# Kernel tuning notes

Hardware: AMD Instinct MI355X
Metric: run time of the kernel (lower is better)

## Reference

```python
import jax, jax.numpy as jnp
import numpy as np

B, N_ATOMS, N_ALIGN = 65536, 128, 64


def setup_inputs() -> dict:
    key = jax.random.key(0)
    k1, k2 = jax.random.split(key)
    traj = jax.random.normal(k1, (B, N_ATOMS, 3), dtype=jnp.float32)
    ref_pos = jax.random.normal(k2, (N_ATOMS, 3), dtype=jnp.float32)
    align_idx = jnp.arange(N_ALIGN, dtype=jnp.int32)  # 0-based (ids - 1)
    return {"traj": traj, "ref_pos": ref_pos, "align_idx": align_idx}


def reference(traj, ref_pos, align_idx):
    # --- __init__: centered reference coordinates of alignment atoms ---
    ref_x = ref_pos[align_idx]                      # [K, 3]
    ref_x = ref_x - jnp.mean(ref_x, axis=0)         # center

    # --- forward: Kabsch alignment per frame ---
    sel = traj[:, align_idx, :]                     # [B, K, 3]
    x_c = jnp.mean(sel, axis=1, keepdims=True)      # [B, 1, 3]
    x_notran = sel - x_c                            # [B, K, 3]
    # xtmp = x_notran^T  -> prod[b] = x_notran[b]^T @ ref_x : [B, 3, 3]
    prod = jnp.einsum('bki,kj->bij', x_notran, ref_x)

    u, s, vh = jnp.linalg.svd(prod)                 # u,vh: [B, 3, 3]
    sign_vec = jnp.sign(jnp.linalg.det(u @ vh))     # [B]
    # diag(1, 1, sign) applied on the right of u
    d = jnp.stack([jnp.ones_like(sign_vec), jnp.ones_like(sign_vec), sign_vec], axis=-1)
    rotate_mat = (u * d[:, None, :]) @ vh           # [B, 3, 3]

    aligned_traj = jnp.matmul(traj - x_c, rotate_mat)  # [B, N, 3]
    return aligned_traj
```

## Files before the change

### kernel.cpp

```cpp
#include <hip/hip_runtime.h>
#include <math.h>

#define NATOMS 128
#define NALIGN 64
#define FPB    32
#define TPB    256

#define JACOBI_ROT(app, aqq, apq, arp, arq, pcol, qcol)                 \
  {                                                                     \
    float _apq = (apq);                                                 \
    if (fabsf(_apq) > 1e-20f) {                                         \
      float _tau = ((aqq) - (app)) / (2.0f * _apq);                     \
      float _t = (_tau >= 0.0f ? 1.0f : -1.0f) /                        \
                 (fabsf(_tau) + sqrtf(1.0f + _tau * _tau));             \
      float _c = rsqrtf(1.0f + _t * _t);                                \
      float _s = _t * _c;                                               \
      (app) -= _t * _apq;                                               \
      (aqq) += _t * _apq;                                               \
      (apq) = 0.0f;                                                     \
      float _rp = (arp), _rq = (arq);                                   \
      (arp) = _c * _rp - _s * _rq;                                      \
      (arq) = _s * _rp + _c * _rq;                                      \
      _Pragma("unroll")                                                 \
      for (int _r = 0; _r < 3; _r++) {                                  \
        float _vp = v[3 * _r + (pcol)], _vq = v[3 * _r + (qcol)];       \
        v[3 * _r + (pcol)] = _c * _vp - _s * _vq;                       \
        v[3 * _r + (qcol)] = _s * _vp + _c * _vq;                       \
      }                                                                 \
    }                                                                   \
  }

__global__ __launch_bounds__(TPB) void align_kernel(
    const float* __restrict__ traj,
    const float* __restrict__ ref_pos,
    const int* __restrict__ align_idx,
    float* __restrict__ out,
    int B)
{
    __shared__ float4 s_ref[NALIGN];
    __shared__ int    s_idx[NALIGN];
    __shared__ __align__(16) float s_mat[FPB][12];

    const int t  = threadIdx.x;
    const int f0 = blockIdx.x * FPB;

    if (t < NALIGN) {
        int idx = align_idx[t];
        s_idx[t] = idx;
        float rx = ref_pos[idx * 3 + 0];
        float ry = ref_pos[idx * 3 + 1];
        float rz = ref_pos[idx * 3 + 2];
        float sx = rx, sy = ry, sz = rz;
        #pragma unroll
        for (int off = 32; off >= 1; off >>= 1) {
            sx += __shfl_xor(sx, off);
            sy += __shfl_xor(sy, off);
            sz += __shfl_xor(sz, off);
        }
        const float inv = 1.0f / (float)NALIGN;
        s_ref[t] = make_float4(rx - sx * inv, ry - sy * inv, rz - sz * inv, 0.0f);
    }
    __syncthreads();

    {
        const int f   = t >> 3;
        const int sub = t & 7;
        const int gf  = f0 + f;
        if (gf < B) {
            const float* fr = traj + (size_t)gf * (NATOMS * 3);
            float px[8], py[8], pz[8];
            float sx = 0.f, sy = 0.f, sz = 0.f;
            #pragma unroll
            for (int i = 0; i < 8; i++) {
                int a   = sub + 8 * i;
                int idx = s_idx[a];
                float x = fr[idx * 3 + 0];
                float y = fr[idx * 3 + 1];
                float z = fr[idx * 3 + 2];
                px[i] = x; py[i] = y; pz[i] = z;
                sx += x; sy += y; sz += z;
            }
            #pragma unroll
            for (int off = 4; off >= 1; off >>= 1) {
                sx += __shfl_xor(sx, off);
                sy += __shfl_xor(sy, off);
                sz += __shfl_xor(sz, off);
            }
            const float inv = 1.0f / (float)NALIGN;
            float xcx = sx * inv, xcy = sy * inv, xcz = sz * inv;

            float c[9] = {0.f,0.f,0.f,0.f,0.f,0.f,0.f,0.f,0.f};
            #pragma unroll
            for (int i = 0; i < 8; i++) {
                int a = sub + 8 * i;
                float4 r = s_ref[a];
                float dx = px[i] - xcx, dy = py[i] - xcy, dz = pz[i] - xcz;
                c[0] += dx * r.x; c[1] += dx * r.y; c[2] += dx * r.z;
                c[3] += dy * r.x; c[4] += dy * r.y; c[5] += dy * r.z;
                c[6] += dz * r.x; c[7] += dz * r.y; c[8] += dz * r.z;
            }
            #pragma unroll
            for (int off = 4; off >= 1; off >>= 1) {
                #pragma unroll
                for (int j = 0; j < 9; j++) c[j] += __shfl_xor(c[j], off);
            }
            if (sub == 0) {
                #pragma unroll
                for (int j = 0; j < 9; j++) s_mat[f][j] = c[j];
                s_mat[f][9]  = xcx;
                s_mat[f][10] = xcy;
                s_mat[f][11] = xcz;
            }
        }
    }
    __syncthreads();

    if (t < FPB && (f0 + t) < B) {
        float m[9];
        #pragma unroll
        for (int j = 0; j < 9; j++) m[j] = s_mat[t][j];

        float a00 = m[0]*m[0] + m[3]*m[3] + m[6]*m[6];
        float a01 = m[0]*m[1] + m[3]*m[4] + m[6]*m[7];
        float a02 = m[0]*m[2] + m[3]*m[5] + m[6]*m[8];
        float a11 = m[1]*m[1] + m[4]*m[4] + m[7]*m[7];
        float a12 = m[1]*m[2] + m[4]*m[5] + m[7]*m[8];
        float a22 = m[2]*m[2] + m[5]*m[5] + m[8]*m[8];

        float v[9] = {1.f,0.f,0.f, 0.f,1.f,0.f, 0.f,0.f,1.f};
        #pragma unroll
        for (int sweep = 0; sweep < 5; sweep++) {
            JACOBI_ROT(a00, a11, a01, a02, a12, 0, 1);
            JACOBI_ROT(a00, a22, a02, a01, a12, 0, 2);
            JACOBI_ROT(a11, a22, a12, a01, a02, 1, 2);
        }

        float dd[3] = {a00, a11, a22};
        #pragma unroll
        for (int pass = 0; pass < 3; pass++) {
            int ii = (pass == 0) ? 0 : (pass == 1) ? 0 : 1;
            int jj = (pass == 0) ? 1 : 2;
            if (dd[ii] < dd[jj]) {
                float tmp = dd[ii]; dd[ii] = dd[jj]; dd[jj] = tmp;
                #pragma unroll
                for (int r = 0; r < 3; r++) {
                    float tv = v[3*r+ii]; v[3*r+ii] = v[3*r+jj]; v[3*r+jj] = tv;
                }
            }
        }

        float v0x = v[0], v0y = v[3], v0z = v[6];
        float v1x = v[1], v1y = v[4], v1z = v[7];
        float v2x = v[2], v2y = v[5], v2z = v[8];

        float u1x = m[0]*v0x + m[1]*v0y + m[2]*v0z;
        float u1y = m[3]*v0x + m[4]*v0y + m[5]*v0z;
        float u1z = m[6]*v0x + m[7]*v0y + m[8]*v0z;
        float n1 = rsqrtf(fmaxf(u1x*u1x + u1y*u1y + u1z*u1z, 1e-30f));
        u1x *= n1; u1y *= n1; u1z *= n1;

        float u2x = m[0]*v1x + m[1]*v1y + m[2]*v1z;
        float u2y = m[3]*v1x + m[4]*v1y + m[5]*v1z;
        float u2z = m[6]*v1x + m[7]*v1y + m[8]*v1z;
        float d12 = u1x*u2x + u1y*u2y + u1z*u2z;
        u2x -= d12 * u1x; u2y -= d12 * u1y; u2z -= d12 * u1z;
        float n2 = rsqrtf(fmaxf(u2x*u2x + u2y*u2y + u2z*u2z, 1e-30f));
        u2x *= n2; u2y *= n2; u2z *= n2;

        float u3x = u1y*u2z - u1z*u2y;
        float u3y = u1z*u2x - u1x*u2z;
        float u3z = u1x*u2y - u1y*u2x;
        float cx = v1y*v2z - v1z*v2y;
        float cy = v1z*v2x - v1x*v2z;
        float cz = v1x*v2y - v1y*v2x;
        float detv = v0x*cx + v0y*cy + v0z*cz;
        float sg = (detv >= 0.f) ? 1.f : -1.f;
        u3x *= sg; u3y *= sg; u3z *= sg;

        s_mat[t][0] = u1x*v0x + u2x*v1x + u3x*v2x;
        s_mat[t][1] = u1x*v0y + u2x*v1y + u3x*v2y;
        s_mat[t][2] = u1x*v0z + u2x*v1z + u3x*v2z;
        s_mat[t][3] = u1y*v0x + u2y*v1x + u3y*v2x;
        s_mat[t][4] = u1y*v0y + u2y*v1y + u3y*v2y;
        s_mat[t][5] = u1y*v0z + u2y*v1z + u3y*v2z;
        s_mat[t][6] = u1z*v0x + u2z*v1x + u3z*v2x;
        s_mat[t][7] = u1z*v0y + u2z*v1y + u3z*v2y;
        s_mat[t][8] = u1z*v0z + u2z*v1z + u3z*v2z;
    }
    __syncthreads();

    #pragma unroll
    for (int i = 0; i < 4; i++) {
        int ab = i * TPB + t;
        int f  = ab >> 5;
        int r  = ab & 31;
        int gf = f0 + f;
        if (gf < B) {
            const float* p = traj + (size_t)gf * (NATOMS * 3) + r * 12;
            float4 q0 = *(const float4*)(p);
            float4 q1 = *(const float4*)(p + 4);
            float4 q2 = *(const float4*)(p + 8);

            float4 Ra = *(const float4*)&s_mat[f][0];
            float4 Rb = *(const float4*)&s_mat[f][4];
            float4 Rc = *(const float4*)&s_mat[f][8];
            float R0 = Ra.x, R1 = Ra.y, R2 = Ra.z, R3 = Ra.w;
            float R4 = Rb.x, R5 = Rb.y, R6 = Rb.z, R7 = Rb.w;
            float R8 = Rc.x, xcx = Rc.y, xcy = Rc.z, xcz = Rc.w;

            float dx, dy, dz;
            dx = q0.x - xcx; dy = q0.y - xcy; dz = q0.z - xcz;
            float o0x = dx*R0 + dy*R3 + dz*R6;
            float o0y = dx*R1 + dy*R4 + dz*R7;
            float o0z = dx*R2 + dy*R5 + dz*R8;
            dx = q0.w - xcx; dy = q1.x - xcy; dz = q1.y - xcz;
            float o1x = dx*R0 + dy*R3 + dz*R6;
            float o1y = dx*R1 + dy*R4 + dz*R7;
            float o1z = dx*R2 + dy*R5 + dz*R8;
            dx = q1.z - xcx; dy = q1.w - xcy; dz = q2.x - xcz;
            float o2x = dx*R0 + dy*R3 + dz*R6;
            float o2y = dx*R1 + dy*R4 + dz*R7;
            float o2z = dx*R2 + dy*R5 + dz*R8;
            dx = q2.y - xcx; dy = q2.z - xcy; dz = q2.w - xcz;
            float o3x = dx*R0 + dy*R3 + dz*R6;
            float o3y = dx*R1 + dy*R4 + dz*R7;
            float o3z = dx*R2 + dy*R5 + dz*R8;

            float* po = out + (size_t)gf * (NATOMS * 3) + r * 12;
            *(float4*)(po)     = make_float4(o0x, o0y, o0z, o1x);
            *(float4*)(po + 4) = make_float4(o1y, o1z, o2x, o2y);
            *(float4*)(po + 8) = make_float4(o2z, o3x, o3y, o3z);
        }
    }
}

extern "C" void kernel_launch(void* const* d_in, const int* in_sizes, int n_in,
                              void* d_out, int out_size, void* d_ws, size_t ws_size,
                              hipStream_t stream) {
    const float* traj      = (const float*)d_in[0];
    const float* ref_pos   = (const float*)d_in[1];
    const int*   align_idx = (const int*)d_in[2];
    float*       out       = (float*)d_out;

    int B = in_sizes[0] / (NATOMS * 3);
    int grid = (B + FPB - 1) / FPB;
    align_kernel<<<grid, TPB, 0, stream>>>(traj, ref_pos, align_idx, out, B);
}
```

Measured before the change: 194.2 us.

## Load each frame once into registers, compute covariance via weighted reference, nontemporal stores

Each frame's full coordinates are now loaded once with coalesced float4 reads into registers, up front. The same registers feed both the covariance and centroid pass and the final rotation pass, which removes the gather of aligned atoms followed by a second global read. The reference is scattered into a per-atom weighted table, with weight 1 for aligned atoms and 0 otherwise, so the centroid and covariance come from uncentered sums over every atom with a 32-lane reduction. Outputs are written with nontemporal stores to avoid polluting the cache. The cost is higher register pressure from holding 48 floats per thread, plus extra FMAs on non-aligned atoms.

```diff
diff --git a/kernel.cpp b/kernel.cpp
--- a/kernel.cpp
+++ b/kernel.cpp
@@ -5,6 +5,8 @@
 #define NALIGN 64
 #define FPB    32
 #define TPB    256
+
+typedef float nfloat4 __attribute__((ext_vector_type(4)));
 
 #define JACOBI_ROT(app, aqq, apq, arp, arq, pcol, qcol)                 \
   {                                                                     \
@@ -37,16 +39,34 @@
     float* __restrict__ out,
     int B)
 {
-    __shared__ float4 s_ref[NALIGN];
-    __shared__ int    s_idx[NALIGN];
+    __shared__ float4 s_wref[NATOMS];
     __shared__ __align__(16) float s_mat[FPB][12];
 
     const int t  = threadIdx.x;
     const int f0 = blockIdx.x * FPB;
-
+    const int r  = t & 31;
+    const int fg = t >> 5;
+
+    float4 q[4][3];
+    int gfv[4];
+    #pragma unroll
+    for (int i = 0; i < 4; i++) {
+        int gf = f0 + i * 8 + fg;
+        gfv[i] = gf;
+        if (gf < B) {
+            const float* p = traj + (size_t)gf * (NATOMS * 3) + r * 12;
+            q[i][0] = *(const float4*)(p);
+            q[i][1] = *(const float4*)(p + 4);
+            q[i][2] = *(const float4*)(p + 8);
+        } else {
+            q[i][0] = q[i][1] = q[i][2] = make_float4(0.f, 0.f, 0.f, 0.f);
+        }
+    }
+
+    if (t < NATOMS) s_wref[t] = make_float4(0.f, 0.f, 0.f, 0.f);
+    __syncthreads();
     if (t < NALIGN) {
         int idx = align_idx[t];
-        s_idx[t] = idx;
         float rx = ref_pos[idx * 3 + 0];
         float ry = ref_pos[idx * 3 + 1];
         float rz = ref_pos[idx * 3 + 2];
@@ -58,59 +78,44 @@
             sz += __shfl_xor(sz, off);
         }
         const float inv = 1.0f / (float)NALIGN;
-        s_ref[t] = make_float4(rx - sx * inv, ry - sy * inv, rz - sz * inv, 0.0f);
-    }
-    __syncthreads();
-
-    {
-        const int f   = t >> 3;
-        const int sub = t & 7;
-        const int gf  = f0 + f;
-        if (gf < B) {
-            const float* fr = traj + (size_t)gf * (NATOMS * 3);
-            float px[8], py[8], pz[8];
-            float sx = 0.f, sy = 0.f, sz = 0.f;
+        s_wref[idx] = make_float4(rx - sx * inv, ry - sy * inv, rz - sz * inv, 1.0f);
+    }
+    __syncthreads();
+
+    #pragma unroll
+    for (int i = 0; i < 4; i++) {
+        float sx = 0.f, sy = 0.f, sz = 0.f;
+        float c[9] = {0.f,0.f,0.f,0.f,0.f,0.f,0.f,0.f,0.f};
+        float ax[4], ay[4], az[4];
+        ax[0]=q[i][0].x; ay[0]=q[i][0].y; az[0]=q[i][0].z;
+        ax[1]=q[i][0].w; ay[1]=q[i][1].x; az[1]=q[i][1].y;
+        ax[2]=q[i][1].z; ay[2]=q[i][1].w; az[2]=q[i][2].x;
+        ax[3]=q[i][2].y; ay[3]=q[i][2].z; az[3]=q[i][2].w;
+        #pragma unroll
+        for (int k = 0; k < 4; k++) {
+            float4 wr = s_wref[r * 4 + k];
+            float x = ax[k], y = ay[k], z = az[k];
+            sx += wr.w * x; sy += wr.w * y; sz += wr.w * z;
+            c[0] += x * wr.x; c[1] += x * wr.y; c[2] += x * wr.z;
+            c[3] += y * wr.x; c[4] += y * wr.y; c[5] += y * wr.z;
+            c[6] += z * wr.x; c[7] += z * wr.y; c[8] += z * wr.z;
+        }
+        #pragma unroll
+        for (int off = 16; off >= 1; off >>= 1) {
+            sx += __shfl_xor(sx, off);
+            sy += __shfl_xor(sy, off);
+            sz += __shfl_xor(sz, off);
             #pragma unroll
-            for (int i = 0; i < 8; i++) {
-                int a   = sub + 8 * i;
-                int idx = s_idx[a];
-                float x = fr[idx * 3 + 0];
-                float y = fr[idx * 3 + 1];
-                float z = fr[idx * 3 + 2];
-                px[i] = x; py[i] = y; pz[i] = z;
-                sx += x; sy += y; sz += z;
-            }
+            for (int j = 0; j < 9; j++) c[j] += __shfl_xor(c[j], off);
+        }
+        if (r == 0 && gfv[i] < B) {
+            int f = i * 8 + fg;
             #pragma unroll
-            for (int off = 4; off >= 1; off >>= 1) {
-                sx += __shfl_xor(sx, off);
-                sy += __shfl_xor(sy, off);
-                sz += __shfl_xor(sz, off);
-            }
+            for (int j = 0; j < 9; j++) s_mat[f][j] = c[j];
             const float inv = 1.0f / (float)NALIGN;
-            float xcx = sx * inv, xcy = sy * inv, xcz = sz * inv;
-
-            float c[9] = {0.f,0.f,0.f,0.f,0.f,0.f,0.f,0.f,0.f};
-            #pragma unroll
-            for (int i = 0; i < 8; i++) {
-                int a = sub + 8 * i;
-                float4 r = s_ref[a];
-                float dx = px[i] - xcx, dy = py[i] - xcy, dz = pz[i] - xcz;
-                c[0] += dx * r.x; c[1] += dx * r.y; c[2] += dx * r.z;
-                c[3] += dy * r.x; c[4] += dy * r.y; c[5] += dy * r.z;
-                c[6] += dz * r.x; c[7] += dz * r.y; c[8] += dz * r.z;
-            }
-            #pragma unroll
-            for (int off = 4; off >= 1; off >>= 1) {
-                #pragma unroll
-                for (int j = 0; j < 9; j++) c[j] += __shfl_xor(c[j], off);
-            }
-            if (sub == 0) {
-                #pragma unroll
-                for (int j = 0; j < 9; j++) s_mat[f][j] = c[j];
-                s_mat[f][9]  = xcx;
-                s_mat[f][10] = xcy;
-                s_mat[f][11] = xcz;
-            }
+            s_mat[f][9]  = sx * inv;
+            s_mat[f][10] = sy * inv;
+            s_mat[f][11] = sz * inv;
         }
     }
     __syncthreads();
@@ -143,8 +148,8 @@
             if (dd[ii] < dd[jj]) {
                 float tmp = dd[ii]; dd[ii] = dd[jj]; dd[jj] = tmp;
                 #pragma unroll
-                for (int r = 0; r < 3; r++) {
-                    float tv = v[3*r+ii]; v[3*r+ii] = v[3*r+jj]; v[3*r+jj] = tv;
+                for (int rr = 0; rr < 3; rr++) {
+                    float tv = v[3*rr+ii]; v[3*rr+ii] = v[3*rr+jj]; v[3*rr+jj] = tv;
                 }
             }
         }
@@ -191,16 +196,9 @@
 
     #pragma unroll
     for (int i = 0; i < 4; i++) {
-        int ab = i * TPB + t;
-        int f  = ab >> 5;
-        int r  = ab & 31;
-        int gf = f0 + f;
+        int gf = gfv[i];
         if (gf < B) {
-            const float* p = traj + (size_t)gf * (NATOMS * 3) + r * 12;
-            float4 q0 = *(const float4*)(p);
-            float4 q1 = *(const float4*)(p + 4);
-            float4 q2 = *(const float4*)(p + 8);
-
+            int f = i * 8 + fg;
             float4 Ra = *(const float4*)&s_mat[f][0];
             float4 Rb = *(const float4*)&s_mat[f][4];
             float4 Rc = *(const float4*)&s_mat[f][8];
@@ -208,6 +206,7 @@
             float R4 = Rb.x, R5 = Rb.y, R6 = Rb.z, R7 = Rb.w;
             float R8 = Rc.x, xcx = Rc.y, xcy = Rc.z, xcz = Rc.w;
 
+            float4 q0 = q[i][0], q1 = q[i][1], q2 = q[i][2];
             float dx, dy, dz;
             dx = q0.x - xcx; dy = q0.y - xcy; dz = q0.z - xcz;
             float o0x = dx*R0 + dy*R3 + dz*R6;
@@ -227,9 +226,12 @@
             float o3z = dx*R2 + dy*R5 + dz*R8;
 
             float* po = out + (size_t)gf * (NATOMS * 3) + r * 12;
-            *(float4*)(po)     = make_float4(o0x, o0y, o0z, o1x);
-            *(float4*)(po + 4) = make_float4(o1y, o1z, o2x, o2y);
-            *(float4*)(po + 8) = make_float4(o2z, o3x, o3y, o3z);
+            nfloat4 w0 = {o0x, o0y, o0z, o1x};
+            nfloat4 w1 = {o1y, o1z, o2x, o2y};
+            nfloat4 w2 = {o2z, o3x, o3y, o3z};
+            __builtin_nontemporal_store(w0, (nfloat4*)(po));
+            __builtin_nontemporal_store(w1, (nfloat4*)(po + 4));
+            __builtin_nontemporal_store(w2, (nfloat4*)(po + 8));
         }
     }
 }
```

Result: slower. 212.6 us (+9.5%).

## Split alignment into rotation and apply kernels with coalesced LDS staging

Applied to the files above, without the earlier changes.

Splits the fused kernel into two. The first stages whole frames through LDS with coalesced float4 loads, computes each frame's rotation and centroid, and writes them to workspace. The second re-reads traj with coalesced loads, applies the rotation through a padded LDS buffer, and writes the output coalesced. This removes the strided gathers and stride-12 float4 accesses, but traj is now read twice from global memory and there is an extra launch. The first kernel also loads all 128 atoms per frame, though only the 64 alignment atoms are used.

```diff
diff --git a/kernel.cpp b/kernel.cpp
--- a/kernel.cpp
+++ b/kernel.cpp
@@ -5,6 +5,7 @@
 #define NALIGN 64
 #define FPB    32
 #define TPB    256
+#define FSTRIDE 97
 
 #define JACOBI_ROT(app, aqq, apq, arp, arq, pcol, qcol)                 \
   {                                                                     \
@@ -30,13 +31,14 @@
     }                                                                   \
   }
 
-__global__ __launch_bounds__(TPB) void align_kernel(
+__global__ __launch_bounds__(TPB) void compute_R_kernel(
     const float* __restrict__ traj,
     const float* __restrict__ ref_pos,
     const int* __restrict__ align_idx,
-    float* __restrict__ out,
+    float* __restrict__ ws,
     int B)
 {
+    __shared__ float4 s_traj[FPB * FSTRIDE];
     __shared__ float4 s_ref[NALIGN];
     __shared__ int    s_idx[NALIGN];
     __shared__ __align__(16) float s_mat[FPB][12];
@@ -60,6 +62,17 @@
         const float inv = 1.0f / (float)NALIGN;
         s_ref[t] = make_float4(rx - sx * inv, ry - sy * inv, rz - sz * inv, 0.0f);
     }
+
+    const float4* g4 = (const float4*)traj + (size_t)f0 * 96;
+    #pragma unroll
+    for (int k = 0; k < 12; k++) {
+        int j = k * TPB + t;
+        int f = j / 96;
+        int p = j - f * 96;
+        if (f0 + f < B) {
+            s_traj[f * FSTRIDE + p] = g4[j];
+        }
+    }
     __syncthreads();
 
     {
@@ -67,7 +80,7 @@
         const int sub = t & 7;
         const int gf  = f0 + f;
         if (gf < B) {
-            const float* fr = traj + (size_t)gf * (NATOMS * 3);
+            const float* fr = (const float*)&s_traj[f * FSTRIDE];
             float px[8], py[8], pz[8];
             float sx = 0.f, sy = 0.f, sz = 0.f;
             #pragma unroll
@@ -143,8 +156,8 @@
             if (dd[ii] < dd[jj]) {
                 float tmp = dd[ii]; dd[ii] = dd[jj]; dd[jj] = tmp;
                 #pragma unroll
-                for (int r = 0; r < 3; r++) {
-                    float tv = v[3*r+ii]; v[3*r+ii] = v[3*r+jj]; v[3*r+jj] = tv;
+                for (int rr = 0; rr < 3; rr++) {
+                    float tv = v[3*rr+ii]; v[3*rr+ii] = v[3*rr+jj]; v[3*rr+jj] = tv;
                 }
             }
         }
@@ -177,36 +190,63 @@
         float sg = (detv >= 0.f) ? 1.f : -1.f;
         u3x *= sg; u3y *= sg; u3z *= sg;
 
-        s_mat[t][0] = u1x*v0x + u2x*v1x + u3x*v2x;
-        s_mat[t][1] = u1x*v0y + u2x*v1y + u3x*v2y;
-        s_mat[t][2] = u1x*v0z + u2x*v1z + u3x*v2z;
-        s_mat[t][3] = u1y*v0x + u2y*v1x + u3y*v2x;
-        s_mat[t][4] = u1y*v0y + u2y*v1y + u3y*v2y;
-        s_mat[t][5] = u1y*v0z + u2y*v1z + u3y*v2z;
-        s_mat[t][6] = u1z*v0x + u2z*v1x + u3z*v2x;
-        s_mat[t][7] = u1z*v0y + u2z*v1y + u3z*v2y;
-        s_mat[t][8] = u1z*v0z + u2z*v1z + u3z*v2z;
-    }
-    __syncthreads();
-
+        float R0 = u1x*v0x + u2x*v1x + u3x*v2x;
+        float R1 = u1x*v0y + u2x*v1y + u3x*v2y;
+        float R2 = u1x*v0z + u2x*v1z + u3x*v2z;
+        float R3 = u1y*v0x + u2y*v1x + u3y*v2x;
+        float R4 = u1y*v0y + u2y*v1y + u3y*v2y;
+        float R5 = u1y*v0z + u2y*v1z + u3y*v2z;
+        float R6 = u1z*v0x + u2z*v1x + u3z*v2x;
+        float R7 = u1z*v0y + u2z*v1y + u3z*v2y;
+        float R8 = u1z*v0z + u2z*v1z + u3z*v2z;
+
+        float4* w4 = (float4*)ws + (size_t)(f0 + t) * 3;
+        w4[0] = make_float4(R0, R1, R2, R3);
+        w4[1] = make_float4(R4, R5, R6, R7);
+        w4[2] = make_float4(R8, s_mat[t][9], s_mat[t][10], s_mat[t][11]);
+    }
+}
+
+__global__ __launch_bounds__(TPB) void apply_kernel(
+    const float* __restrict__ traj,
+    const float* __restrict__ ws,
+    float* __restrict__ out,
+    int B)
+{
+    __shared__ float4 s_buf[8 * FSTRIDE];
+    __shared__ float  s_R[8 * 12];
+
+    const int t = threadIdx.x;
+    const size_t tile = blockIdx.x;
+    const int fbase = (int)tile * 8;
+    const float4* in4 = (const float4*)traj + tile * 768;
+    float4* out4 = (float4*)out + tile * 768;
+
+    if (t < 96) {
+        int f = t / 12;
+        if (fbase + f < B) s_R[t] = ws[(size_t)(fbase) * 12 + t];
+    }
     #pragma unroll
-    for (int i = 0; i < 4; i++) {
-        int ab = i * TPB + t;
-        int f  = ab >> 5;
-        int r  = ab & 31;
-        int gf = f0 + f;
-        if (gf < B) {
-            const float* p = traj + (size_t)gf * (NATOMS * 3) + r * 12;
-            float4 q0 = *(const float4*)(p);
-            float4 q1 = *(const float4*)(p + 4);
-            float4 q2 = *(const float4*)(p + 8);
-
-            float4 Ra = *(const float4*)&s_mat[f][0];
-            float4 Rb = *(const float4*)&s_mat[f][4];
-            float4 Rc = *(const float4*)&s_mat[f][8];
-            float R0 = Ra.x, R1 = Ra.y, R2 = Ra.z, R3 = Ra.w;
-            float R4 = Rb.x, R5 = Rb.y, R6 = Rb.z, R7 = Rb.w;
-            float R8 = Rc.x, xcx = Rc.y, xcy = Rc.z, xcz = Rc.w;
+    for (int k = 0; k < 3; k++) {
+        int j = k * TPB + t;
+        int f = j / 96;
+        int p = j - f * 96;
+        if (fbase + f < B) s_buf[f * FSTRIDE + p] = in4[j];
+    }
+    __syncthreads();
+
+    {
+        const int f = t >> 5;
+        const int r = t & 31;
+        if (fbase + f < B) {
+            float4 q0 = s_buf[f * FSTRIDE + 3 * r + 0];
+            float4 q1 = s_buf[f * FSTRIDE + 3 * r + 1];
+            float4 q2 = s_buf[f * FSTRIDE + 3 * r + 2];
+
+            const float* Rp = &s_R[f * 12];
+            float R0 = Rp[0], R1 = Rp[1], R2 = Rp[2], R3 = Rp[3];
+            float R4 = Rp[4], R5 = Rp[5], R6 = Rp[6], R7 = Rp[7];
+            float R8 = Rp[8], xcx = Rp[9], xcy = Rp[10], xcz = Rp[11];
 
             float dx, dy, dz;
             dx = q0.x - xcx; dy = q0.y - xcy; dz = q0.z - xcz;
@@ -226,11 +266,19 @@
             float o3y = dx*R1 + dy*R4 + dz*R7;
             float o3z = dx*R2 + dy*R5 + dz*R8;
 
-            float* po = out + (size_t)gf * (NATOMS * 3) + r * 12;
-            *(float4*)(po)     = make_float4(o0x, o0y, o0z, o1x);
-            *(float4*)(po + 4) = make_float4(o1y, o1z, o2x, o2y);
-            *(float4*)(po + 8) = make_float4(o2z, o3x, o3y, o3z);
-        }
+            s_buf[f * FSTRIDE + 3 * r + 0] = make_float4(o0x, o0y, o0z, o1x);
+            s_buf[f * FSTRIDE + 3 * r + 1] = make_float4(o1y, o1z, o2x, o2y);
+            s_buf[f * FSTRIDE + 3 * r + 2] = make_float4(o2z, o3x, o3y, o3z);
+        }
+    }
+    __syncthreads();
+
+    #pragma unroll
+    for (int k = 0; k < 3; k++) {
+        int j = k * TPB + t;
+        int f = j / 96;
+        int p = j - f * 96;
+        if (fbase + f < B) out4[j] = s_buf[f * FSTRIDE + p];
     }
 }
 
@@ -241,8 +289,11 @@
     const float* ref_pos   = (const float*)d_in[1];
     const int*   align_idx = (const int*)d_in[2];
     float*       out       = (float*)d_out;
+    float*       ws        = (float*)d_ws;
 
     int B = in_sizes[0] / (NATOMS * 3);
-    int grid = (B + FPB - 1) / FPB;
-    align_kernel<<<grid, TPB, 0, stream>>>(traj, ref_pos, align_idx, out, B);
+    int grid1 = (B + FPB - 1) / FPB;
+    compute_R_kernel<<<grid1, TPB, 0, stream>>>(traj, ref_pos, align_idx, ws, B);
+    int grid2 = (B + 7) / 8;
+    apply_kernel<<<grid2, TPB, 0, stream>>>(traj, ws, out, B);
 }
```

Measured after the change: 210.7 us. +8.5%, slower.

## Stage each frame's trajectory in padded shared memory and read it once

Applied to the files above, without the earlier changes.

The trajectory tile for each block is now loaded once from global memory into a padded LDS buffer (stride 97 float4 per frame) with coalesced float4 loads. Both the covariance pass and the final rotation pass read from that buffer instead of going to global memory twice. Frames per block drop from 32 to 16 to fit the roughly 25 KB buffer. The covariance is now accumulated from raw coordinates in a single pass without subtracting the centroid first, which relies on the reference coordinates being centered and adds some floating-point cancellation risk. The price is fewer frames per block and heavier LDS use, which may lower occupancy.

```diff
diff --git a/kernel.cpp b/kernel.cpp
--- a/kernel.cpp
+++ b/kernel.cpp
@@ -3,8 +3,9 @@
 
 #define NATOMS 128
 #define NALIGN 64
-#define FPB    32
+#define FPB    16
 #define TPB    256
+#define FSTRIDE 97
 
 #define JACOBI_ROT(app, aqq, apq, arp, arq, pcol, qcol)                 \
   {                                                                     \
@@ -37,6 +38,7 @@
     float* __restrict__ out,
     int B)
 {
+    __shared__ float4 s_traj[FPB * FSTRIDE];
     __shared__ float4 s_ref[NALIGN];
     __shared__ int    s_idx[NALIGN];
     __shared__ __align__(16) float s_mat[FPB][12];
@@ -60,56 +62,53 @@
         const float inv = 1.0f / (float)NALIGN;
         s_ref[t] = make_float4(rx - sx * inv, ry - sy * inv, rz - sz * inv, 0.0f);
     }
+
+    const float4* g4 = (const float4*)traj + (size_t)f0 * 96;
+    #pragma unroll
+    for (int k = 0; k < 6; k++) {
+        int j = k * TPB + t;
+        int f = j / 96;
+        int p = j - f * 96;
+        if (f0 + f < B) s_traj[f * FSTRIDE + p] = g4[j];
+    }
     __syncthreads();
 
     {
-        const int f   = t >> 3;
-        const int sub = t & 7;
+        const int f   = t >> 4;
+        const int sub = t & 15;
         const int gf  = f0 + f;
         if (gf < B) {
-            const float* fr = traj + (size_t)gf * (NATOMS * 3);
-            float px[8], py[8], pz[8];
+            const float* fr = (const float*)&s_traj[f * FSTRIDE];
             float sx = 0.f, sy = 0.f, sz = 0.f;
+            float c[9] = {0.f,0.f,0.f,0.f,0.f,0.f,0.f,0.f,0.f};
             #pragma unroll
-            for (int i = 0; i < 8; i++) {
-                int a   = sub + 8 * i;
+            for (int i = 0; i < 4; i++) {
+                int a   = sub + 16 * i;
                 int idx = s_idx[a];
                 float x = fr[idx * 3 + 0];
                 float y = fr[idx * 3 + 1];
                 float z = fr[idx * 3 + 2];
-                px[i] = x; py[i] = y; pz[i] = z;
+                float4 rr = s_ref[a];
                 sx += x; sy += y; sz += z;
+                c[0] += x * rr.x; c[1] += x * rr.y; c[2] += x * rr.z;
+                c[3] += y * rr.x; c[4] += y * rr.y; c[5] += y * rr.z;
+                c[6] += z * rr.x; c[7] += z * rr.y; c[8] += z * rr.z;
             }
             #pragma unroll
-            for (int off = 4; off >= 1; off >>= 1) {
+            for (int off = 8; off >= 1; off >>= 1) {
                 sx += __shfl_xor(sx, off);
                 sy += __shfl_xor(sy, off);
                 sz += __shfl_xor(sz, off);
-            }
-            const float inv = 1.0f / (float)NALIGN;
-            float xcx = sx * inv, xcy = sy * inv, xcz = sz * inv;
-
-            float c[9] = {0.f,0.f,0.f,0.f,0.f,0.f,0.f,0.f,0.f};
-            #pragma unroll
-            for (int i = 0; i < 8; i++) {
-                int a = sub + 8 * i;
-                float4 r = s_ref[a];
-                float dx = px[i] - xcx, dy = py[i] - xcy, dz = pz[i] - xcz;
-                c[0] += dx * r.x; c[1] += dx * r.y; c[2] += dx * r.z;
-                c[3] += dy * r.x; c[4] += dy * r.y; c[5] += dy * r.z;
-                c[6] += dz * r.x; c[7] += dz * r.y; c[8] += dz * r.z;
-            }
-            #pragma unroll
-            for (int off = 4; off >= 1; off >>= 1) {
                 #pragma unroll
                 for (int j = 0; j < 9; j++) c[j] += __shfl_xor(c[j], off);
             }
             if (sub == 0) {
                 #pragma unroll
                 for (int j = 0; j < 9; j++) s_mat[f][j] = c[j];
-                s_mat[f][9]  = xcx;
-                s_mat[f][10] = xcy;
-                s_mat[f][11] = xcz;
+                const float inv = 1.0f / (float)NALIGN;
+                s_mat[f][9]  = sx * inv;
+                s_mat[f][10] = sy * inv;
+                s_mat[f][11] = sz * inv;
             }
         }
     }
@@ -143,8 +142,8 @@
             if (dd[ii] < dd[jj]) {
                 float tmp = dd[ii]; dd[ii] = dd[jj]; dd[jj] = tmp;
                 #pragma unroll
-                for (int r = 0; r < 3; r++) {
-                    float tv = v[3*r+ii]; v[3*r+ii] = v[3*r+jj]; v[3*r+jj] = tv;
+                for (int rr = 0; rr < 3; rr++) {
+                    float tv = v[3*rr+ii]; v[3*rr+ii] = v[3*rr+jj]; v[3*rr+jj] = tv;
                 }
             }
         }
@@ -190,16 +189,15 @@
     __syncthreads();
 
     #pragma unroll
-    for (int i = 0; i < 4; i++) {
-        int ab = i * TPB + t;
-        int f  = ab >> 5;
-        int r  = ab & 31;
+    for (int w = 0; w < 2; w++) {
+        int j  = w * TPB + t;
+        int f  = j >> 5;
+        int r  = j & 31;
         int gf = f0 + f;
         if (gf < B) {
-            const float* p = traj + (size_t)gf * (NATOMS * 3) + r * 12;
-            float4 q0 = *(const float4*)(p);
-            float4 q1 = *(const float4*)(p + 4);
-            float4 q2 = *(const float4*)(p + 8);
+            float4 q0 = s_traj[f * FSTRIDE + 3 * r + 0];
+            float4 q1 = s_traj[f * FSTRIDE + 3 * r + 1];
+            float4 q2 = s_traj[f * FSTRIDE + 3 * r + 2];
 
             float4 Ra = *(const float4*)&s_mat[f][0];
             float4 Rb = *(const float4*)&s_mat[f][4];
```

Result: slower. 199.1 us (+2.5%).
